# Kernel optimization log

Hardware: AMD Instinct MI355X
Metric: run time of the kernel (lower is better)

The kernel has to match this reference:

```python
import jax, jax.numpy as jnp
import numpy as np

D = 256       # d_model
HEADS = 8     # n_heads
PTS = 4       # n_points
FF = 1024     # dim_feedforward
HD = D // HEADS
B, Q = 8, 900
HH, WW = 100, 100


def setup_inputs() -> dict:
    key = jax.random.key(0)
    ks = iter(jax.random.split(key, 40))
    p = lambda shape: jax.random.normal(next(ks), shape, dtype=jnp.float32) * 0.02
    inp = {
        "tgt": jax.random.normal(next(ks), (B, Q, D), dtype=jnp.float32),
        "memory": jax.random.normal(next(ks), (B, HH * WW, D), dtype=jnp.float32),
        "H": HH,
        "W": WW,
        # self-attention (nn.MultiheadAttention) params
        "in_proj_w": p((3 * D, D)), "in_proj_b": p((3 * D,)),
        "out_proj_w": p((D, D)), "out_proj_b": p((D,)),
        # layer norms
        "norm1_s": jnp.ones((D,)), "norm1_b": jnp.zeros((D,)),
        "norm2_s": jnp.ones((D,)), "norm2_b": jnp.zeros((D,)),
        "norm3_s": jnp.ones((D,)), "norm3_b": jnp.zeros((D,)),
        # deformable cross-attention params
        "vproj_w": p((D, D)), "vproj_b": p((D,)),
        "offs_w": p((HEADS * PTS * 2, D)), "offs_b": p((HEADS * PTS * 2,)),
        "attw_w": p((HEADS * PTS, D)), "attw_b": p((HEADS * PTS,)),
        "ref_w": p((2, D)), "ref_b": p((2,)),
        "cout_w": p((D, D)), "cout_b": p((D,)),
        # FFN params
        "ffn_w1": p((FF, D)), "ffn_b1": p((FF,)),
        "ffn_w2": p((D, FF)), "ffn_b2": p((D,)),
    }
    return inp


def _layer_norm(x, s, b):
    m = jnp.mean(x, -1, keepdims=True)
    v = jnp.mean((x - m) ** 2, -1, keepdims=True)
    return (x - m) * jax.lax.rsqrt(v + 1e-5) * s + b


def _mha(x, wi, bi, wo, bo):
    b, q, _ = x.shape
    qkv = x @ wi.T + bi
    qh, kh, vh = jnp.split(qkv, 3, axis=-1)
    qh = qh.reshape(b, q, HEADS, HD).transpose(0, 2, 1, 3)
    kh = kh.reshape(b, q, HEADS, HD).transpose(0, 2, 1, 3)
    vh = vh.reshape(b, q, HEADS, HD).transpose(0, 2, 1, 3)
    att = jax.nn.softmax(jnp.einsum('bhqd,bhkd->bhqk', qh, kh) / np.float32(np.sqrt(HD)), axis=-1)
    o = jnp.einsum('bhqk,bhkd->bhqd', att, vh).transpose(0, 2, 1, 3).reshape(b, q, D)
    return o @ wo.T + bo


def _deform_attn(q, mem, H, W, vproj_w, vproj_b, offs_w, offs_b, attw_w, attw_b,
                 ref_w, ref_b, cout_w, cout_b):
    b, nq, _ = q.shape
    # per-query normalized reference points (x, y) in [0,1]
    ref = jax.nn.sigmoid(q @ ref_w.T + ref_b)                         # [B,Q,2]
    offs = (q @ offs_w.T + offs_b).reshape(b, nq, HEADS, PTS, 2)      # [B,Q,h,p,2]
    attw = jax.nn.softmax((q @ attw_w.T + attw_b).reshape(b, nq, HEADS, PTS), axis=-1)
    val = (mem @ vproj_w.T + vproj_b).reshape(b, H * W, HEADS, HD).transpose(0, 2, 1, 3)  # [B,h,HW,hd]
    wh = jnp.array([W, H], dtype=q.dtype)
    loc = ref[:, :, None, None, :] + offs / wh                        # normalized sampling loc
    x = loc[..., 0] * W - 0.5                                         # pixel coords (align_corners=False)
    y = loc[..., 1] * H - 0.5
    x0 = jnp.floor(x); y0 = jnp.floor(y)
    lx = x - x0; ly = y - y0
    x0i = x0.astype(jnp.int32); y0i = y0.astype(jnp.int32)

    def gather(xi, yi):
        valid = ((xi >= 0) & (xi < W) & (yi >= 0) & (yi < H)).astype(q.dtype)
        idx = jnp.clip(yi, 0, H - 1) * W + jnp.clip(xi, 0, W - 1)     # [B,Q,h,p]
        idxt = idx.transpose(0, 2, 1, 3).reshape(b, HEADS, nq * PTS, 1)
        g = jnp.take_along_axis(val, idxt, axis=2)                    # [B,h,Q*p,hd]
        g = g.reshape(b, HEADS, nq, PTS, HD).transpose(0, 2, 1, 3, 4)  # [B,Q,h,p,hd]
        return g * valid[..., None]

    samp = (gather(x0i, y0i) * ((1 - lx) * (1 - ly))[..., None]
            + gather(x0i + 1, y0i) * (lx * (1 - ly))[..., None]
            + gather(x0i, y0i + 1) * ((1 - lx) * ly)[..., None]
            + gather(x0i + 1, y0i + 1) * (lx * ly)[..., None])        # [B,Q,h,p,hd]
    out = jnp.sum(samp * attw[..., None], axis=3).reshape(b, nq, D)
    return out @ cout_w.T + cout_b


def reference(tgt, memory, H, W, in_proj_w, in_proj_b, out_proj_w, out_proj_b,
              norm1_s, norm1_b, norm2_s, norm2_b, norm3_s, norm3_b,
              vproj_w, vproj_b, offs_w, offs_b, attw_w, attw_b, ref_w, ref_b,
              cout_w, cout_b, ffn_w1, ffn_b1, ffn_w2, ffn_b2):
    t2 = _mha(tgt, in_proj_w, in_proj_b, out_proj_w, out_proj_b)
    t = _layer_norm(tgt + t2, norm1_s, norm1_b)
    t2 = _deform_attn(t, memory, H, W, vproj_w, vproj_b, offs_w, offs_b,
                      attw_w, attw_b, ref_w, ref_b, cout_w, cout_b)
    t = _layer_norm(t + t2, norm2_s, norm2_b)
    f = jnp.maximum(t @ ffn_w1.T + ffn_b1, 0) @ ffn_w2.T + ffn_b2
    return _layer_norm(t + f, norm3_s, norm3_b)
```

## Files before the change

### kernel.cpp

```cpp
#include <hip/hip_runtime.h>
#include <hip/hip_bf16.h>

typedef __hip_bfloat16 bf16;
typedef __attribute__((ext_vector_type(8))) short short8;
typedef __attribute__((ext_vector_type(4))) float f32x4;

#define BB 8
#define QQ 900
#define DD 256
#define NH 8
#define HD 32
#define NPTS 4
#define FFD 1024
#define HH 100
#define WW2 100
#define HWTOT 10000

#define QT 64
#define KTC 128
#define NCHUNK ((QQ + KTC - 1) / KTC)
#define QB 4

__device__ inline float tofloat(float x) { return x; }
__device__ inline float tofloat(bf16 x) { return __bfloat162float(x); }
__device__ inline float bf2f(unsigned short u) {
    return __uint_as_float(((unsigned int)u) << 16);
}
__device__ inline void storev(bf16* p, float v) { *p = __float2bfloat16(v); }
__device__ inline void storev(float* p, float v) { *p = v; }

__global__ void pack_kernel(const float* __restrict__ in_proj_w, const float* __restrict__ out_proj_w,
                            const float* __restrict__ cout_w, const float* __restrict__ ffn_w1,
                            const float* __restrict__ ffn_w2, const float* __restrict__ vproj_w,
                            const float* __restrict__ offs_w, const float* __restrict__ attw_w,
                            const float* __restrict__ ref_w, const float* __restrict__ offs_b,
                            const float* __restrict__ attw_b, const float* __restrict__ ref_b,
                            const float* __restrict__ tgt, bf16* __restrict__ wpk,
                            bf16* __restrict__ tgtb, float* __restrict__ dbias) {
    const int idx = blockIdx.x * 256 + threadIdx.x;
    const int TOT = 950272 + 1843200 + 128;
    if (idx >= TOT) return;
    if (idx < 196608) {
        wpk[idx] = __float2bfloat16(in_proj_w[idx]);
    } else if (idx < 262144) {
        wpk[idx] = __float2bfloat16(out_proj_w[idx - 196608]);
    } else if (idx < 327680) {
        wpk[idx] = __float2bfloat16(cout_w[idx - 262144]);
    } else if (idx < 589824) {
        wpk[idx] = __float2bfloat16(ffn_w1[idx - 327680]);
    } else if (idx < 851968) {
        wpk[idx] = __float2bfloat16(ffn_w2[idx - 589824]);
    } else if (idx < 917504) {
        wpk[idx] = __float2bfloat16(vproj_w[idx - 851968]);
    } else if (idx < 950272) {
        const int j = idx - 917504;
        const int r = j >> 8, c = j & 255;
        float v = 0.f;
        if (r < 64) v = offs_w[r * 256 + c];
        else if (r < 96) v = attw_w[(r - 64) * 256 + c];
        else if (r < 98) v = ref_w[(r - 96) * 256 + c];
        wpk[idx] = __float2bfloat16(v);
    } else if (idx < 950272 + 1843200) {
        const int j = idx - 950272;
        tgtb[j] = __float2bfloat16(tgt[j]);
    } else {
        const int j = idx - (950272 + 1843200);
        float v = 0.f;
        if (j < 64) v = offs_b[j];
        else if (j < 96) v = attw_b[j - 64];
        else if (j < 98) v = ref_b[j - 96];
        dbias[j] = v;
    }
}

template <int ACT, typename OT>
__global__ __launch_bounds__(256) void gemm_mfma_kernel(const bf16* __restrict__ A,
                                                        const bf16* __restrict__ W,
                                                        const float* __restrict__ bias,
                                                        OT* __restrict__ C, int M, int N, int K) {
    __shared__ unsigned short As[64][56];
    __shared__ unsigned short Bs[64][56];
    const int bm = blockIdx.y * 64, bn = blockIdx.x * 64;
    const int tid = threadIdx.x;
    const int lane = tid & 63, wave = tid >> 6;
    const int sr = tid >> 2, sc = (tid & 3) * 8;
    f32x4 acc[4] = {{0.f, 0.f, 0.f, 0.f}, {0.f, 0.f, 0.f, 0.f},
                    {0.f, 0.f, 0.f, 0.f}, {0.f, 0.f, 0.f, 0.f}};
    const uint4 zero4 = {0u, 0u, 0u, 0u};
    for (int k0 = 0; k0 < K; k0 += 32) {
        __syncthreads();
        {
            const int arow = bm + sr;
            uint4 a4 = (arow < M) ? *(const uint4*)(A + (size_t)arow * K + k0 + sc) : zero4;
            *(uint4*)&As[sr][sc] = a4;
            const int wrow = bn + sr;
            uint4 b4 = (wrow < N) ? *(const uint4*)(W + (size_t)wrow * K + k0 + sc) : zero4;
            *(uint4*)&Bs[sr][sc] = b4;
        }
        __syncthreads();
        const short8 af = *(const short8*)&As[wave * 16 + (lane & 15)][(lane >> 4) * 8];
#pragma unroll
        for (int ct = 0; ct < 4; ++ct) {
            const short8 bf = *(const short8*)&Bs[ct * 16 + (lane & 15)][(lane >> 4) * 8];
            acc[ct] = __builtin_amdgcn_mfma_f32_16x16x32_bf16(af, bf, acc[ct], 0, 0, 0);
        }
    }
#pragma unroll
    for (int ct = 0; ct < 4; ++ct) {
        const int col = bn + ct * 16 + (lane & 15);
        const float bv = bias[col];
#pragma unroll
        for (int r = 0; r < 4; ++r) {
            const int row = bm + wave * 16 + (lane >> 4) * 4 + r;
            if (row < M) {
                float v = acc[ct][r] + bv;
                if (ACT == 1) v = fmaxf(v, 0.f);
                storev(&C[(size_t)row * N + col], v);
            }
        }
    }
}

__global__ __launch_bounds__(256) void mha_mfma_kernel(const bf16* __restrict__ qkv,
                                                       bf16* __restrict__ o) {
    const int qt = blockIdx.x, h = blockIdx.y, b = blockIdx.z;
    const int tid = threadIdx.x;
    const int lane = tid & 63, wave = tid >> 6;
    const int l15 = lane & 15, g = lane >> 4;
    __shared__ unsigned short Kls[KTC][40];
    __shared__ bf16 Vt[HD][136];
    __shared__ bf16 Pls[4][16][136];
    const size_t base = (size_t)b * QQ * 768;
    const int q0 = qt * QT;

    short8 qa = {0, 0, 0, 0, 0, 0, 0, 0};
    {
        const int qg = q0 + wave * 16 + l15;
        if (qg < QQ)
            qa = *(const short8*)(qkv + base + (size_t)qg * 768 + h * HD + g * 8);
    }
    f32x4 accO[2] = {{0.f, 0.f, 0.f, 0.f}, {0.f, 0.f, 0.f, 0.f}};
    float m_run[4], l_run[4];
#pragma unroll
    for (int r = 0; r < 4; ++r) {
        m_run[r] = -1e30f;
        l_run[r] = 0.f;
    }
    const float scale = 0.17677669529663687f;
    const uint4 zero4 = {0u, 0u, 0u, 0u};

    for (int c = 0; c < NCHUNK; ++c) {
        const int k0 = c * KTC;
        __syncthreads();
        {
            const int part = tid & 3, kr = tid >> 2;
#pragma unroll
            for (int pass = 0; pass < 2; ++pass) {
                const int krr = kr + pass * 64;
                const int kg = k0 + krr;
                uint4 kv = (kg < QQ)
                    ? *(const uint4*)(qkv + base + (size_t)kg * 768 + DD + h * HD + part * 8)
                    : zero4;
                *(uint4*)&Kls[krr][part * 8] = kv;
            }
        }
        {
            const int kr = tid >> 1, ch0 = (tid & 1) * 16;
            const int kg = k0 + kr;
            uint4 v0 = zero4, v1 = zero4;
            if (kg < QQ) {
                const bf16* pv = qkv + base + (size_t)kg * 768 + 2 * DD + h * HD + ch0;
                v0 = *(const uint4*)pv;
                v1 = *(const uint4*)(pv + 8);
            }
            const unsigned short* u0 = (const unsigned short*)&v0;
            const unsigned short* u1 = (const unsigned short*)&v1;
#pragma unroll
            for (int j = 0; j < 8; ++j) {
                ((unsigned short*)&Vt[ch0 + j][kr])[0] = u0[j];
                ((unsigned short*)&Vt[ch0 + 8 + j][kr])[0] = u1[j];
            }
        }
        __syncthreads();

        f32x4 s[8];
#pragma unroll
        for (int t = 0; t < 8; ++t) {
            const short8 kb = *(const short8*)&Kls[t * 16 + l15][g * 8];
            const f32x4 z = {0.f, 0.f, 0.f, 0.f};
            s[t] = __builtin_amdgcn_mfma_f32_16x16x32_bf16(qa, kb, z, 0, 0, 0);
        }
        float mx[4] = {-1e30f, -1e30f, -1e30f, -1e30f};
#pragma unroll
        for (int t = 0; t < 8; ++t) {
            const bool cv = (k0 + t * 16 + l15) < QQ;
#pragma unroll
            for (int r = 0; r < 4; ++r) {
                const float v = cv ? s[t][r] * scale : -1e30f;
                s[t][r] = v;
                mx[r] = fmaxf(mx[r], v);
            }
        }
#pragma unroll
        for (int r = 0; r < 4; ++r) {
            mx[r] = fmaxf(mx[r], __shfl_xor(mx[r], 1));
            mx[r] = fmaxf(mx[r], __shfl_xor(mx[r], 2));
            mx[r] = fmaxf(mx[r], __shfl_xor(mx[r], 4));
            mx[r] = fmaxf(mx[r], __shfl_xor(mx[r], 8));
        }
        float alpha[4], rs[4];
#pragma unroll
        for (int r = 0; r < 4; ++r) {
            const float mn = fmaxf(m_run[r], mx[r]);
            alpha[r] = __expf(m_run[r] - mn);
            m_run[r] = mn;
            rs[r] = 0.f;
        }
#pragma unroll
        for (int t = 0; t < 8; ++t) {
#pragma unroll
            for (int r = 0; r < 4; ++r) {
                const float p = __expf(s[t][r] - m_run[r]);
                rs[r] += p;
                Pls[wave][g * 4 + r][t * 16 + l15] = __float2bfloat16(p);
            }
        }
#pragma unroll
        for (int r = 0; r < 4; ++r) {
            rs[r] += __shfl_xor(rs[r], 1);
            rs[r] += __shfl_xor(rs[r], 2);
            rs[r] += __shfl_xor(rs[r], 4);
            rs[r] += __shfl_xor(rs[r], 8);
            l_run[r] = l_run[r] * alpha[r] + rs[r];
        }
#pragma unroll
        for (int t2 = 0; t2 < 2; ++t2)
#pragma unroll
            for (int r = 0; r < 4; ++r) accO[t2][r] *= alpha[r];
#pragma unroll
        for (int s4 = 0; s4 < 4; ++s4) {
            const short8 pa = *(const short8*)&Pls[wave][l15][s4 * 32 + g * 8];
#pragma unroll
            for (int t2 = 0; t2 < 2; ++t2) {
                const short8 vb = *(const short8*)&Vt[t2 * 16 + l15][s4 * 32 + g * 8];
                accO[t2] = __builtin_amdgcn_mfma_f32_16x16x32_bf16(pa, vb, accO[t2], 0, 0, 0);
            }
        }
    }
#pragma unroll
    for (int r = 0; r < 4; ++r) {
        const int row = q0 + wave * 16 + g * 4 + r;
        if (row < QQ) {
            const float inv = 1.f / l_run[r];
#pragma unroll
            for (int t2 = 0; t2 < 2; ++t2) {
                storev(&o[((size_t)b * QQ + row) * DD + h * HD + t2 * 16 + l15],
                       accO[t2][r] * inv);
            }
        }
    }
}

template <typename TR, typename TO>
__global__ void add_ln_kernel(const TR* __restrict__ resid, const bf16* __restrict__ y,
                              const float* __restrict__ g, const float* __restrict__ bta,
                              TO* __restrict__ out) {
    const int row = blockIdx.x;
    const int tid = threadIdx.x;
    __shared__ float red[256];
    const size_t idx = (size_t)row * DD + tid;
    float v = tofloat(resid[idx]) + tofloat(y[idx]);
    red[tid] = v;
    __syncthreads();
    for (int s = 128; s > 0; s >>= 1) {
        if (tid < s) red[tid] += red[tid + s];
        __syncthreads();
    }
    const float mean = red[0] * (1.f / DD);
    __syncthreads();
    const float d = v - mean;
    red[tid] = d * d;
    __syncthreads();
    for (int s = 128; s > 0; s >>= 1) {
        if (tid < s) red[tid] += red[tid + s];
        __syncthreads();
    }
    const float rstd = rsqrtf(red[0] * (1.f / DD) + 1e-5f);
    storev(&out[idx], d * rstd * g[tid] + bta[tid]);
}

__global__ __launch_bounds__(256) void deform_kernel(
    const float* __restrict__ dots, const float* __restrict__ mem,
    const bf16* __restrict__ vwpk, const float* __restrict__ vproj_b,
    bf16* __restrict__ samp) {
    const int qt = blockIdx.x, b = blockIdx.y;
    const int tid = threadIdx.x;
    const int q0 = qt * QB;
    __shared__ int sidx[QB][32][4];
    __shared__ float swt[QB][32][4];
    __shared__ float wsum[QB][NH];
    __shared__ float G[QB * NH * DD];

    if (tid < 128) {
        const int q = tid >> 5, hp = tid & 31;
        const float* dr = dots + ((size_t)b * QQ + q0 + q) * 128;
        const float ox = dr[hp * 2], oy = dr[hp * 2 + 1];
        float ad = dr[64 + hp];
        const float rx = dr[96], ry = dr[97];
        float mx = ad;
        mx = fmaxf(mx, __shfl_xor(mx, 1));
        mx = fmaxf(mx, __shfl_xor(mx, 2));
        float e = __expf(ad - mx);
        float sm = e;
        sm += __shfl_xor(sm, 1);
        sm += __shfl_xor(sm, 2);
        const float a = e / sm;
        const float refx = 1.f / (1.f + __expf(-rx));
        const float refy = 1.f / (1.f + __expf(-ry));
        const float x = (refx + ox * (1.f / WW2)) * WW2 - 0.5f;
        const float y = (refy + oy * (1.f / HH)) * HH - 0.5f;
        const float x0f = floorf(x), y0f = floorf(y);
        const float lx = x - x0f, ly = y - y0f;
        const int x0 = (int)x0f, y0 = (int)y0f;
        const float cw[4] = {(1 - lx) * (1 - ly), lx * (1 - ly), (1 - lx) * ly, lx * ly};
        const int cx[4] = {x0, x0 + 1, x0, x0 + 1};
        const int cy[4] = {y0, y0, y0 + 1, y0 + 1};
        float cs = 0.f;
#pragma unroll
        for (int cc = 0; cc < 4; ++cc) {
            const bool valid = cx[cc] >= 0 && cx[cc] < WW2 && cy[cc] >= 0 && cy[cc] < HH;
            const int xi = min(max(cx[cc], 0), WW2 - 1);
            const int yi = min(max(cy[cc], 0), HH - 1);
            sidx[q][hp][cc] = yi * WW2 + xi;
            const float w = valid ? a * cw[cc] : 0.f;
            swt[q][hp][cc] = w;
            cs += w;
        }
        cs += __shfl_xor(cs, 1);
        cs += __shfl_xor(cs, 2);
        if ((hp & 3) == 0) wsum[q][hp >> 2] = cs;
    }
    __syncthreads();

    {
        const int q = tid >> 6, c4o = (tid & 63) * 4;
        const float* mb = mem + (size_t)b * HWTOT * DD;
        float4* Gp = (float4*)G;
#pragma unroll
        for (int h = 0; h < NH; ++h) {
            float4 acc = {0.f, 0.f, 0.f, 0.f};
#pragma unroll
            for (int p = 0; p < NPTS; ++p) {
                const int hp = h * NPTS + p;
#pragma unroll
                for (int cc = 0; cc < 4; ++cc) {
                    const float w = swt[q][hp][cc];
                    const float4 v = *(const float4*)(mb + (size_t)sidx[q][hp][cc] * DD + c4o);
                    acc.x += w * v.x;
                    acc.y += w * v.y;
                    acc.z += w * v.z;
                    acc.w += w * v.w;
                }
            }
            Gp[(q * NH + h) * 64 + (tid & 63)] = acc;
        }
    }
    __syncthreads();

    {
        const int ch = tid, h = ch >> 5;
        const bf16* wr = vwpk + (size_t)ch * DD;
        const float bv = vproj_b[ch];
        float acc[QB];
#pragma unroll
        for (int q = 0; q < QB; ++q) acc[q] = wsum[q][h] * bv;
        for (int k = 0; k < DD; k += 8) {
            const uint4 u = *(const uint4*)(wr + k);
            const unsigned short* us = (const unsigned short*)&u;
            float wf[8];
#pragma unroll
            for (int j = 0; j < 8; ++j) wf[j] = bf2f(us[j]);
#pragma unroll
            for (int q = 0; q < QB; ++q) {
                const float* gq = &G[(q * NH + h) * DD + k];
#pragma unroll
                for (int j = 0; j < 8; ++j) acc[q] += gq[j] * wf[j];
            }
        }
#pragma unroll
        for (int q = 0; q < QB; ++q) {
            storev(&samp[((size_t)b * QQ + q0 + q) * DD + ch], acc[q]);
        }
    }
}

extern "C" void kernel_launch(void* const* d_in, const int* in_sizes, int n_in,
                              void* d_out, int out_size, void* d_ws, size_t ws_size,
                              hipStream_t stream) {
    const float* tgt = (const float*)d_in[0];
    const float* memory = (const float*)d_in[1];
    const float* in_proj_w = (const float*)d_in[4];
    const float* in_proj_b = (const float*)d_in[5];
    const float* out_proj_w = (const float*)d_in[6];
    const float* out_proj_b = (const float*)d_in[7];
    const float* norm1_s = (const float*)d_in[8];
    const float* norm1_b = (const float*)d_in[9];
    const float* norm2_s = (const float*)d_in[10];
    const float* norm2_b = (const float*)d_in[11];
    const float* norm3_s = (const float*)d_in[12];
    const float* norm3_b = (const float*)d_in[13];
    const float* vproj_w = (const float*)d_in[14];
    const float* vproj_b = (const float*)d_in[15];
    const float* offs_w = (const float*)d_in[16];
    const float* offs_b = (const float*)d_in[17];
    const float* attw_w = (const float*)d_in[18];
    const float* attw_b = (const float*)d_in[19];
    const float* ref_w = (const float*)d_in[20];
    const float* ref_b = (const float*)d_in[21];
    const float* cout_w = (const float*)d_in[22];
    const float* cout_b = (const float*)d_in[23];
    const float* ffn_w1 = (const float*)d_in[24];
    const float* ffn_b1 = (const float*)d_in[25];
    const float* ffn_w2 = (const float*)d_in[26];
    const float* ffn_b2 = (const float*)d_in[27];

    const int M = BB * QQ;
    bf16* ws = (bf16*)d_ws;
    size_t off = 0;
    bf16* qkv = ws + off;  off += (size_t)M * 768;
    bf16* o = ws + off;    off += (size_t)M * DD;
    bf16* t1 = ws + off;   off += (size_t)M * DD;
    bf16* tmp = ws + off;  off += (size_t)M * DD;
    bf16* ffh = ws + off;  off += (size_t)M * FFD;
    bf16* tgtb = ws + off; off += (size_t)M * DD;
    bf16* wpk = ws + off;  off += 950272;
    float* dbias = (float*)(ws + off);
    bf16* samp = o;
    bf16* t2n = qkv;
    float* dots = (float*)ffh;

    bf16* w_in = wpk;
    bf16* w_out = wpk + 196608;
    bf16* w_cout = wpk + 262144;
    bf16* w_ffn1 = wpk + 327680;
    bf16* w_ffn2 = wpk + 589824;
    bf16* w_vproj = wpk + 851968;
    bf16* w_dots = wpk + 917504;

    const int MT = (M + 63) / 64;

    pack_kernel<<<(950272 + 1843200 + 128 + 255) / 256, 256, 0, stream>>>(
        in_proj_w, out_proj_w, cout_w, ffn_w1, ffn_w2, vproj_w, offs_w, attw_w, ref_w,
        offs_b, attw_b, ref_b, tgt, wpk, tgtb, dbias);
    gemm_mfma_kernel<0, bf16><<<dim3(12, MT), 256, 0, stream>>>(tgtb, w_in, in_proj_b, qkv,
                                                                M, 768, DD);
    mha_mfma_kernel<<<dim3((QQ + QT - 1) / QT, NH, BB), 256, 0, stream>>>(qkv, o);
    gemm_mfma_kernel<0, bf16><<<dim3(4, MT), 256, 0, stream>>>(o, w_out, out_proj_b, tmp,
                                                               M, DD, DD);
    add_ln_kernel<float, bf16><<<M, 256, 0, stream>>>(tgt, tmp, norm1_s, norm1_b, t1);
    gemm_mfma_kernel<0, float><<<dim3(2, MT), 256, 0, stream>>>(t1, w_dots, dbias, dots,
                                                                M, 128, DD);
    deform_kernel<<<dim3(QQ / QB, BB), 256, 0, stream>>>(dots, memory, w_vproj, vproj_b, samp);
    gemm_mfma_kernel<0, bf16><<<dim3(4, MT), 256, 0, stream>>>(samp, w_cout, cout_b, tmp,
                                                               M, DD, DD);
    add_ln_kernel<bf16, bf16><<<M, 256, 0, stream>>>(t1, tmp, norm2_s, norm2_b, t2n);
    gemm_mfma_kernel<1, bf16><<<dim3(16, MT), 256, 0, stream>>>(t2n, w_ffn1, ffn_b1, ffh,
                                                                M, FFD, DD);
    gemm_mfma_kernel<0, bf16><<<dim3(4, MT), 256, 0, stream>>>(ffh, w_ffn2, ffn_b2, tmp,
                                                               M, DD, FFD);
    add_ln_kernel<bf16, float><<<M, 256, 0, stream>>>(t2n, tmp, norm3_s, norm3_b,
                                                      (float*)d_out);
}
```

Baseline: 385.2 us.

## Precompute value projection over memory and gather projected bf16 values per head

Moves the value projection out of the per-query deformable kernel into a single MFMA GEMM over all memory tokens, producing bf16 projected values. The gather kernel then reads only each head's 32-channel slice per sampling corner and sums weighted samples, skipping the per-query CUDA-core matvec. The GEMM is also retiled to 128-row blocks and can load fp32 A directly, removing the separate tgt conversion pass. It adds a full pass over memory (reading fp32, writing bf16) and extra workspace.

```diff
diff --git a/kernel.cpp b/kernel.cpp
--- a/kernel.cpp
+++ b/kernel.cpp
@@ -19,7 +19,7 @@
 #define QT 64
 #define KTC 128
 #define NCHUNK ((QQ + KTC - 1) / KTC)
-#define QB 4
+#define GQB 8
 
 __device__ inline float tofloat(float x) { return x; }
 __device__ inline float tofloat(bf16 x) { return __bfloat162float(x); }
@@ -28,6 +28,10 @@
 }
 __device__ inline void storev(bf16* p, float v) { *p = __float2bfloat16(v); }
 __device__ inline void storev(float* p, float v) { *p = v; }
+__device__ inline unsigned short f2bu(float v) {
+    bf16 t = __float2bfloat16(v);
+    return *(unsigned short*)&t;
+}
 
 __global__ void pack_kernel(const float* __restrict__ in_proj_w, const float* __restrict__ out_proj_w,
                             const float* __restrict__ cout_w, const float* __restrict__ ffn_w1,
@@ -35,10 +39,9 @@
                             const float* __restrict__ offs_w, const float* __restrict__ attw_w,
                             const float* __restrict__ ref_w, const float* __restrict__ offs_b,
                             const float* __restrict__ attw_b, const float* __restrict__ ref_b,
-                            const float* __restrict__ tgt, bf16* __restrict__ wpk,
-                            bf16* __restrict__ tgtb, float* __restrict__ dbias) {
+                            bf16* __restrict__ wpk, float* __restrict__ dbias) {
     const int idx = blockIdx.x * 256 + threadIdx.x;
-    const int TOT = 950272 + 1843200 + 128;
+    const int TOT = 950272 + 128;
     if (idx >= TOT) return;
     if (idx < 196608) {
         wpk[idx] = __float2bfloat16(in_proj_w[idx]);
@@ -60,11 +63,8 @@
         else if (r < 96) v = attw_w[(r - 64) * 256 + c];
         else if (r < 98) v = ref_w[(r - 96) * 256 + c];
         wpk[idx] = __float2bfloat16(v);
-    } else if (idx < 950272 + 1843200) {
+    } else {
         const int j = idx - 950272;
-        tgtb[j] = __float2bfloat16(tgt[j]);
-    } else {
-        const int j = idx - (950272 + 1843200);
         float v = 0.f;
         if (j < 64) v = offs_b[j];
         else if (j < 96) v = attw_b[j - 64];
@@ -73,52 +73,81 @@
     }
 }
 
-template <int ACT, typename OT>
-__global__ __launch_bounds__(256) void gemm_mfma_kernel(const bf16* __restrict__ A,
+__device__ inline void stage8(unsigned short* dst, const bf16* A, size_t off, bool ok) {
+    const uint4 z = {0u, 0u, 0u, 0u};
+    *(uint4*)dst = ok ? *(const uint4*)((const unsigned short*)A + off) : z;
+}
+__device__ inline void stage8(unsigned short* dst, const float* A, size_t off, bool ok) {
+    if (ok) {
+        const float4 f0 = *(const float4*)(A + off);
+        const float4 f1 = *(const float4*)(A + off + 4);
+        dst[0] = f2bu(f0.x); dst[1] = f2bu(f0.y); dst[2] = f2bu(f0.z); dst[3] = f2bu(f0.w);
+        dst[4] = f2bu(f1.x); dst[5] = f2bu(f1.y); dst[6] = f2bu(f1.z); dst[7] = f2bu(f1.w);
+    } else {
+        const uint4 z = {0u, 0u, 0u, 0u};
+        *(uint4*)dst = z;
+    }
+}
+
+template <int ACT, typename TA, typename OT>
+__global__ __launch_bounds__(256) void gemm_mfma_kernel(const TA* __restrict__ A,
                                                         const bf16* __restrict__ W,
                                                         const float* __restrict__ bias,
                                                         OT* __restrict__ C, int M, int N, int K) {
-    __shared__ unsigned short As[64][56];
-    __shared__ unsigned short Bs[64][56];
-    const int bm = blockIdx.y * 64, bn = blockIdx.x * 64;
+    __shared__ unsigned short As[128][40];
+    __shared__ unsigned short Bs[64][40];
+    const int bm = blockIdx.y * 128, bn = blockIdx.x * 64;
     const int tid = threadIdx.x;
     const int lane = tid & 63, wave = tid >> 6;
-    const int sr = tid >> 2, sc = (tid & 3) * 8;
-    f32x4 acc[4] = {{0.f, 0.f, 0.f, 0.f}, {0.f, 0.f, 0.f, 0.f},
-                    {0.f, 0.f, 0.f, 0.f}, {0.f, 0.f, 0.f, 0.f}};
-    const uint4 zero4 = {0u, 0u, 0u, 0u};
+    const int l15 = lane & 15, g = lane >> 4;
+    const f32x4 zf = {0.f, 0.f, 0.f, 0.f};
+    f32x4 acc[2][4];
+#pragma unroll
+    for (int rt = 0; rt < 2; ++rt)
+#pragma unroll
+        for (int ct = 0; ct < 4; ++ct) acc[rt][ct] = zf;
+
     for (int k0 = 0; k0 < K; k0 += 32) {
         __syncthreads();
+#pragma unroll
+        for (int pass = 0; pass < 2; ++pass) {
+            const int c = tid + pass * 256;
+            const int r = c >> 2, col = (c & 3) * 8;
+            const int arow = bm + r;
+            stage8(&As[r][col], A, (size_t)arow * K + k0 + col, arow < M);
+        }
         {
-            const int arow = bm + sr;
-            uint4 a4 = (arow < M) ? *(const uint4*)(A + (size_t)arow * K + k0 + sc) : zero4;
-            *(uint4*)&As[sr][sc] = a4;
-            const int wrow = bn + sr;
-            uint4 b4 = (wrow < N) ? *(const uint4*)(W + (size_t)wrow * K + k0 + sc) : zero4;
-            *(uint4*)&Bs[sr][sc] = b4;
-        }
-        __syncthreads();
-        const short8 af = *(const short8*)&As[wave * 16 + (lane & 15)][(lane >> 4) * 8];
+            const int r = tid >> 2, col = (tid & 3) * 8;
+            const int wrow = bn + r;
+            stage8(&Bs[r][col], W, (size_t)wrow * K + k0 + col, wrow < N);
+        }
+        __syncthreads();
+        short8 af[2];
+        af[0] = *(const short8*)&As[wave * 32 + l15][g * 8];
+        af[1] = *(const short8*)&As[wave * 32 + 16 + l15][g * 8];
 #pragma unroll
         for (int ct = 0; ct < 4; ++ct) {
-            const short8 bf = *(const short8*)&Bs[ct * 16 + (lane & 15)][(lane >> 4) * 8];
-            acc[ct] = __builtin_amdgcn_mfma_f32_16x16x32_bf16(af, bf, acc[ct], 0, 0, 0);
-        }
-    }
-#pragma unroll
-    for (int ct = 0; ct < 4; ++ct) {
-        const int col = bn + ct * 16 + (lane & 15);
-        const float bv = bias[col];
-#pragma unroll
-        for (int r = 0; r < 4; ++r) {
-            const int row = bm + wave * 16 + (lane >> 4) * 4 + r;
-            if (row < M) {
-                float v = acc[ct][r] + bv;
-                if (ACT == 1) v = fmaxf(v, 0.f);
-                storev(&C[(size_t)row * N + col], v);
-            }
-        }
-    }
+            const short8 bf = *(const short8*)&Bs[ct * 16 + l15][g * 8];
+            acc[0][ct] = __builtin_amdgcn_mfma_f32_16x16x32_bf16(af[0], bf, acc[0][ct], 0, 0, 0);
+            acc[1][ct] = __builtin_amdgcn_mfma_f32_16x16x32_bf16(af[1], bf, acc[1][ct], 0, 0, 0);
+        }
+    }
+#pragma unroll
+    for (int rt = 0; rt < 2; ++rt)
+#pragma unroll
+        for (int ct = 0; ct < 4; ++ct) {
+            const int col = bn + ct * 16 + l15;
+            const float bv = bias[col];
+#pragma unroll
+            for (int r = 0; r < 4; ++r) {
+                const int row = bm + wave * 32 + rt * 16 + g * 4 + r;
+                if (row < M) {
+                    float v = acc[rt][ct][r] + bv;
+                    if (ACT == 1) v = fmaxf(v, 0.f);
+                    storev(&C[(size_t)row * N + col], v);
+                }
+            }
+        }
 }
 
 __global__ __launch_bounds__(256) void mha_mfma_kernel(const bf16* __restrict__ qkv,
@@ -289,28 +318,28 @@
     storev(&out[idx], d * rstd * g[tid] + bta[tid]);
 }
 
-__global__ __launch_bounds__(256) void deform_kernel(
-    const float* __restrict__ dots, const float* __restrict__ mem,
-    const bf16* __restrict__ vwpk, const float* __restrict__ vproj_b,
-    bf16* __restrict__ samp) {
-    const int qt = blockIdx.x, b = blockIdx.y;
+__global__ __launch_bounds__(256) void deform_gather_kernel(const float* __restrict__ dots,
+                                                            const bf16* __restrict__ val,
+                                                            bf16* __restrict__ samp) {
+    const int b = blockIdx.y;
+    const int q0 = blockIdx.x * GQB;
     const int tid = threadIdx.x;
-    const int q0 = qt * QB;
-    __shared__ int sidx[QB][32][4];
-    __shared__ float swt[QB][32][4];
-    __shared__ float wsum[QB][NH];
-    __shared__ float G[QB * NH * DD];
-
-    if (tid < 128) {
-        const int q = tid >> 5, hp = tid & 31;
-        const float* dr = dots + ((size_t)b * QQ + q0 + q) * 128;
+    const int q = tid >> 5, hp = tid & 31, h = hp >> 2;
+    const int qg = q0 + q;
+    __shared__ float Gs[GQB][32][36];
+    float accv[32];
+#pragma unroll
+    for (int j = 0; j < 32; ++j) accv[j] = 0.f;
+
+    if (qg < QQ) {
+        const float* dr = dots + ((size_t)b * QQ + qg) * 128;
         const float ox = dr[hp * 2], oy = dr[hp * 2 + 1];
-        float ad = dr[64 + hp];
+        const float ad = dr[64 + hp];
         const float rx = dr[96], ry = dr[97];
         float mx = ad;
         mx = fmaxf(mx, __shfl_xor(mx, 1));
         mx = fmaxf(mx, __shfl_xor(mx, 2));
-        float e = __expf(ad - mx);
+        const float e = __expf(ad - mx);
         float sm = e;
         sm += __shfl_xor(sm, 1);
         sm += __shfl_xor(sm, 2);
@@ -325,71 +354,56 @@
         const float cw[4] = {(1 - lx) * (1 - ly), lx * (1 - ly), (1 - lx) * ly, lx * ly};
         const int cx[4] = {x0, x0 + 1, x0, x0 + 1};
         const int cy[4] = {y0, y0, y0 + 1, y0 + 1};
-        float cs = 0.f;
+        const bf16* vb = val + (size_t)b * HWTOT * DD + h * HD;
 #pragma unroll
         for (int cc = 0; cc < 4; ++cc) {
             const bool valid = cx[cc] >= 0 && cx[cc] < WW2 && cy[cc] >= 0 && cy[cc] < HH;
-            const int xi = min(max(cx[cc], 0), WW2 - 1);
-            const int yi = min(max(cy[cc], 0), HH - 1);
-            sidx[q][hp][cc] = yi * WW2 + xi;
             const float w = valid ? a * cw[cc] : 0.f;
-            swt[q][hp][cc] = w;
-            cs += w;
-        }
-        cs += __shfl_xor(cs, 1);
-        cs += __shfl_xor(cs, 2);
-        if ((hp & 3) == 0) wsum[q][hp >> 2] = cs;
+            if (w != 0.f) {
+                const int xi = min(max(cx[cc], 0), WW2 - 1);
+                const int yi = min(max(cy[cc], 0), HH - 1);
+                const bf16* p = vb + (size_t)(yi * WW2 + xi) * DD;
+                const uint4 u0 = *(const uint4*)p;
+                const uint4 u1 = *(const uint4*)(p + 8);
+                const uint4 u2 = *(const uint4*)(p + 16);
+                const uint4 u3 = *(const uint4*)(p + 24);
+                const unsigned short* s0 = (const unsigned short*)&u0;
+                const unsigned short* s1 = (const unsigned short*)&u1;
+                const unsigned short* s2 = (const unsigned short*)&u2;
+                const unsigned short* s3 = (const unsigned short*)&u3;
+#pragma unroll
+                for (int j = 0; j < 8; ++j) {
+                    accv[j] += w * bf2f(s0[j]);
+                    accv[8 + j] += w * bf2f(s1[j]);
+                    accv[16 + j] += w * bf2f(s2[j]);
+                    accv[24 + j] += w * bf2f(s3[j]);
+                }
+            }
+        }
+    }
+#pragma unroll
+    for (int j4 = 0; j4 < 8; ++j4) {
+        float4 t = {accv[j4 * 4], accv[j4 * 4 + 1], accv[j4 * 4 + 2], accv[j4 * 4 + 3]};
+        *(float4*)&Gs[q][hp][j4 * 4] = t;
     }
     __syncthreads();
-
     {
-        const int q = tid >> 6, c4o = (tid & 63) * 4;
-        const float* mb = mem + (size_t)b * HWTOT * DD;
-        float4* Gp = (float4*)G;
-#pragma unroll
-        for (int h = 0; h < NH; ++h) {
-            float4 acc = {0.f, 0.f, 0.f, 0.f};
-#pragma unroll
-            for (int p = 0; p < NPTS; ++p) {
-                const int hp = h * NPTS + p;
-#pragma unroll
-                for (int cc = 0; cc < 4; ++cc) {
-                    const float w = swt[q][hp][cc];
-                    const float4 v = *(const float4*)(mb + (size_t)sidx[q][hp][cc] * DD + c4o);
-                    acc.x += w * v.x;
-                    acc.y += w * v.y;
-                    acc.z += w * v.z;
-                    acc.w += w * v.w;
-                }
-            }
-            Gp[(q * NH + h) * 64 + (tid & 63)] = acc;
-        }
-    }
-    __syncthreads();
-
-    {
-        const int ch = tid, h = ch >> 5;
-        const bf16* wr = vwpk + (size_t)ch * DD;
-        const float bv = vproj_b[ch];
-        float acc[QB];
-#pragma unroll
-        for (int q = 0; q < QB; ++q) acc[q] = wsum[q][h] * bv;
-        for (int k = 0; k < DD; k += 8) {
-            const uint4 u = *(const uint4*)(wr + k);
-            const unsigned short* us = (const unsigned short*)&u;
-            float wf[8];
-#pragma unroll
-            for (int j = 0; j < 8; ++j) wf[j] = bf2f(us[j]);
-#pragma unroll
-            for (int q = 0; q < QB; ++q) {
-                const float* gq = &G[(q * NH + h) * DD + k];
-#pragma unroll
-                for (int j = 0; j < 8; ++j) acc[q] += gq[j] * wf[j];
-            }
-        }
-#pragma unroll
-        for (int q = 0; q < QB; ++q) {
-            storev(&samp[((size_t)b * QQ + q0 + q) * DD + ch], acc[q]);
+        const int q2 = tid >> 5, idx5 = tid & 31;
+        const int h2 = idx5 >> 2, cg = idx5 & 3;
+        if (q0 + q2 < QQ) {
+            float s[8] = {0.f, 0.f, 0.f, 0.f, 0.f, 0.f, 0.f, 0.f};
+#pragma unroll
+            for (int p = 0; p < 4; ++p) {
+                const float4 a0 = *(const float4*)&Gs[q2][h2 * 4 + p][cg * 8];
+                const float4 a1 = *(const float4*)&Gs[q2][h2 * 4 + p][cg * 8 + 4];
+                s[0] += a0.x; s[1] += a0.y; s[2] += a0.z; s[3] += a0.w;
+                s[4] += a1.x; s[5] += a1.y; s[6] += a1.z; s[7] += a1.w;
+            }
+            unsigned short outp[8];
+#pragma unroll
+            for (int j = 0; j < 8; ++j) outp[j] = f2bu(s[j]);
+            bf16* op = samp + ((size_t)b * QQ + q0 + q2) * DD + h2 * HD + cg * 8;
+            *(uint4*)op = *(uint4*)outp;
         }
     }
 }
@@ -432,9 +446,9 @@
     bf16* t1 = ws + off;   off += (size_t)M * DD;
     bf16* tmp = ws + off;  off += (size_t)M * DD;
     bf16* ffh = ws + off;  off += (size_t)M * FFD;
-    bf16* tgtb = ws + off; off += (size_t)M * DD;
     bf16* wpk = ws + off;  off += 950272;
-    float* dbias = (float*)(ws + off);
+    float* dbias = (float*)(ws + off); off += 256;
+    bf16* val = ws + off;  off += (size_t)BB * HWTOT * DD;
     bf16* samp = o;
     bf16* t2n = qkv;
     float* dots = (float*)ffh;
@@ -447,27 +461,29 @@
     bf16* w_vproj = wpk + 851968;
     bf16* w_dots = wpk + 917504;
 
-    const int MT = (M + 63) / 64;
-
-    pack_kernel<<<(950272 + 1843200 + 128 + 255) / 256, 256, 0, stream>>>(
+    const int MT = (M + 127) / 128;
+
+    pack_kernel<<<(950272 + 128 + 255) / 256, 256, 0, stream>>>(
         in_proj_w, out_proj_w, cout_w, ffn_w1, ffn_w2, vproj_w, offs_w, attw_w, ref_w,
-        offs_b, attw_b, ref_b, tgt, wpk, tgtb, dbias);
-    gemm_mfma_kernel<0, bf16><<<dim3(12, MT), 256, 0, stream>>>(tgtb, w_in, in_proj_b, qkv,
-                                                                M, 768, DD);
+        offs_b, attw_b, ref_b, wpk, dbias);
+    gemm_mfma_kernel<0, float, bf16><<<dim3(4, (BB * HWTOT + 127) / 128), 256, 0, stream>>>(
+        memory, w_vproj, vproj_b, val, BB * HWTOT, DD, DD);
+    gemm_mfma_kernel<0, float, bf16><<<dim3(12, MT), 256, 0, stream>>>(tgt, w_in, in_proj_b,
+                                                                       qkv, M, 768, DD);
     mha_mfma_kernel<<<dim3((QQ + QT - 1) / QT, NH, BB), 256, 0, stream>>>(qkv, o);
-    gemm_mfma_kernel<0, bf16><<<dim3(4, MT), 256, 0, stream>>>(o, w_out, out_proj_b, tmp,
-                                                               M, DD, DD);
+    gemm_mfma_kernel<0, bf16, bf16><<<dim3(4, MT), 256, 0, stream>>>(o, w_out, out_proj_b,
+                                                                     tmp, M, DD, DD);
     add_ln_kernel<float, bf16><<<M, 256, 0, stream>>>(tgt, tmp, norm1_s, norm1_b, t1);
-    gemm_mfma_kernel<0, float><<<dim3(2, MT), 256, 0, stream>>>(t1, w_dots, dbias, dots,
-                                                                M, 128, DD);
-    deform_kernel<<<dim3(QQ / QB, BB), 256, 0, stream>>>(dots, memory, w_vproj, vproj_b, samp);
-    gemm_mfma_kernel<0, bf16><<<dim3(4, MT), 256, 0, stream>>>(samp, w_cout, cout_b, tmp,
-                                                               M, DD, DD);
+    gemm_mfma_kernel<0, bf16, float><<<dim3(2, MT), 256, 0, stream>>>(t1, w_dots, dbias,
+                                                                      dots, M, 128, DD);
+    deform_gather_kernel<<<dim3((QQ + GQB - 1) / GQB, BB), 256, 0, stream>>>(dots, val, samp);
+    gemm_mfma_kernel<0, bf16, bf16><<<dim3(4, MT), 256, 0, stream>>>(samp, w_cout, cout_b,
+                                                                     tmp, M, DD, DD);
     add_ln_kernel<bf16, bf16><<<M, 256, 0, stream>>>(t1, tmp, norm2_s, norm2_b, t2n);
-    gemm_mfma_kernel<1, bf16><<<dim3(16, MT), 256, 0, stream>>>(t2n, w_ffn1, ffn_b1, ffh,
-                                                                M, FFD, DD);
-    gemm_mfma_kernel<0, bf16><<<dim3(4, MT), 256, 0, stream>>>(ffh, w_ffn2, ffn_b2, tmp,
-                                                               M, DD, FFD);
+    gemm_mfma_kernel<1, bf16, bf16><<<dim3(16, MT), 256, 0, stream>>>(t2n, w_ffn1, ffn_b1,
+                                                                      ffh, M, FFD, DD);
+    gemm_mfma_kernel<0, bf16, bf16><<<dim3(4, MT), 256, 0, stream>>>(ffh, w_ffn2, ffn_b2,
+                                                                     tmp, M, DD, FFD);
     add_ln_kernel<bf16, float><<<M, 256, 0, stream>>>(t2n, tmp, norm3_s, norm3_b,
                                                       (float*)d_out);
 }
```

Measured after the change: 439.9 us. 1.14x slower.
